# Kernel optimization log

Measured on AMD Instinct MI355X. Metric: run time of the kernel, lower is better.

Reference implementation:

```python
import jax, jax.numpy as jnp
import numpy as np

N = 100000
E = 1600000
IN_DIM, HIDDEN, OUT_DIM, HEADS = 256, 128, 64, 2
NEG_SLOPE = 0.2


def setup_inputs() -> dict:
    key = jax.random.key(0)
    ks = jax.random.split(key, 10)
    inv = lambda d: 1.0 / np.sqrt(d)
    return {
        "x": jax.random.normal(ks[0], (N, IN_DIM), dtype=jnp.float32),
        "edge_index": jax.random.randint(ks[1], (2, E), 0, N, dtype=jnp.int64),
        "W1": jax.random.normal(ks[2], (IN_DIM, HEADS * HIDDEN), dtype=jnp.float32) * inv(IN_DIM),
        "att_src1": jax.random.normal(ks[3], (HEADS, HIDDEN), dtype=jnp.float32) * inv(HIDDEN),
        "att_dst1": jax.random.normal(ks[4], (HEADS, HIDDEN), dtype=jnp.float32) * inv(HIDDEN),
        "b1": jnp.zeros((HIDDEN,), dtype=jnp.float32),
        "W2": jax.random.normal(ks[5], (HIDDEN, OUT_DIM), dtype=jnp.float32) * inv(HIDDEN),
        "att_src2": jax.random.normal(ks[6], (1, OUT_DIM), dtype=jnp.float32) * inv(OUT_DIM),
        "att_dst2": jax.random.normal(ks[7], (1, OUT_DIM), dtype=jnp.float32) * inv(OUT_DIM),
        "b2": jnp.zeros((OUT_DIM,), dtype=jnp.float32),
    }


def gat_conv(x, W, att_src, att_dst, bias, src, dst, heads, ch):
    # Linear transform: [N, H, C]
    h = (x @ W).reshape(N, heads, ch)
    # Per-node attention logits: [N, H]
    a_s = jnp.einsum("nhc,hc->nh", h, att_src)
    a_d = jnp.einsum("nhc,hc->nh", h, att_dst)
    # Edge-wise scores (self-loops already in src/dst): [E', H]
    e = jax.nn.leaky_relu(a_s[src] + a_d[dst], NEG_SLOPE)
    # Segment softmax over incoming edges of each dst node
    m = jax.ops.segment_max(e, dst, num_segments=N)
    alpha = jnp.exp(e - m[dst])
    denom = jax.ops.segment_sum(alpha, dst, num_segments=N)
    alpha = alpha / denom[dst]
    # Weighted scatter-add aggregation: [N, H, C]
    out = jax.ops.segment_sum(alpha[:, :, None] * h[src], dst, num_segments=N)
    # concat=False -> mean over heads, then bias
    return out.mean(axis=1) + bias


def reference(x, edge_index, W1, att_src1, att_dst1, b1, W2, att_src2, att_dst2, b2):
    # PyG GATConv default: add self-loops
    loop = jnp.arange(N, dtype=edge_index.dtype)
    src = jnp.concatenate([edge_index[0], loop])
    dst = jnp.concatenate([edge_index[1], loop])
    h = gat_conv(x, W1, att_src1, att_dst1, b1, src, dst, HEADS, HIDDEN)
    h = jax.nn.relu(h)  # dropout is identity in eval mode
    out = gat_conv(h, W2, att_src2, att_dst2, b2, src, dst, 1, OUT_DIM)
    return out
```

## Files before the change

### kernel.cpp

```cpp
#include <hip/hip_runtime.h>
#include <hip/hip_bf16.h>
#include <cstdint>
#include <cstddef>

#define IN_D 256
#define HID 128
#define OUT_D 64
#define NSLOPE 0.2f
#define SBCAP 20480

typedef __attribute__((ext_vector_type(8))) short bf16x8;
typedef __attribute__((ext_vector_type(4))) float f32x4;
typedef __attribute__((ext_vector_type(8))) unsigned short u16x8;
typedef unsigned short u16;

static inline int cdiv(long long a, long long b) { return (int)((a + b - 1) / b); }

__device__ __forceinline__ float lrelu(float v) { return v >= 0.f ? v : NSLOPE * v; }
__device__ __forceinline__ int imin(int a, int b) { return a < b ? a : b; }

__device__ __forceinline__ u16 f2bf(float f) {
  unsigned u = __float_as_uint(f);
  return (u16)((u + 0x7FFFu + ((u >> 16) & 1u)) >> 16);
}
__device__ __forceinline__ float bf2f(u16 h) {
  return __uint_as_float((unsigned)h << 16);
}

__global__ void k_prep(const float* __restrict__ W1, u16* __restrict__ WThi,
                       u16* __restrict__ WTlo, const float* __restrict__ W2,
                       u16* __restrict__ W2Thi, u16* __restrict__ W2Tlo) {
  int idx = blockIdx.x * 256 + threadIdx.x;
  if (idx < IN_D * IN_D) {
    int k = idx >> 8, n = idx & 255;
    float f = W1[idx];
    u16 h = f2bf(f);
    WThi[n * IN_D + k] = h;
    WTlo[n * IN_D + k] = f2bf(f - bf2f(h));
  }
  int idx2 = idx - IN_D * IN_D;
  if (idx2 >= 0 && idx2 < HID * OUT_D) {
    int k = idx2 >> 6, n = idx2 & 63;
    float f = W2[idx2];
    u16 h = f2bf(f);
    W2Thi[n * HID + k] = h;
    W2Tlo[n * HID + k] = f2bf(f - bf2f(h));
  }
}

__launch_bounds__(256)
__global__ void k_sort1(const int* __restrict__ ei, int E,
                        int* __restrict__ sbCount, int2* __restrict__ st1) {
  __shared__ int hist[128], gb[128], cur[128];
  int tid = threadIdx.x;
  if (tid < 128) hist[tid] = 0;
  __syncthreads();
  int base = blockIdx.x * 2048 + tid;
  int sv[8], dv[8]; bool vv[8];
  #pragma unroll
  for (int q = 0; q < 8; ++q) {
    int i = base + q * 256;
    vv[q] = i < E;
    int ic = vv[q] ? i : 0;
    sv[q] = ei[ic];
    dv[q] = ei[E + ic];
  }
  #pragma unroll
  for (int q = 0; q < 8; ++q)
    if (vv[q]) atomicAdd(&hist[dv[q] >> 10], 1);
  __syncthreads();
  if (tid < 128) {
    int h = hist[tid];
    gb[tid] = h ? atomicAdd(&sbCount[tid], h) : 0;
    cur[tid] = 0;
  }
  __syncthreads();
  #pragma unroll
  for (int q = 0; q < 8; ++q)
    if (vv[q]) {
      int sb = dv[q] >> 10;
      int r = atomicAdd(&cur[sb], 1);
      int slot = gb[sb] + r;
      if (slot < SBCAP) st1[(size_t)sb * SBCAP + slot] = make_int2(sv[q], dv[q]);
    }
}

__launch_bounds__(256)
__global__ void k_sort2(const int* __restrict__ sbCount, const int2* __restrict__ st1,
                        int* __restrict__ ro, int* __restrict__ col, int N) {
  __shared__ int hist2[1024], pref[1024], cur[1024];
  __shared__ int sc[256];
  __shared__ int gbaseS, cntS;
  int tid = threadIdx.x;
  int sb = blockIdx.x;
  int nb0 = sb << 10;
  if (tid == 0) {
    int g = 0;
    for (int b = 0; b < sb; ++b) g += imin(sbCount[b], SBCAP);
    gbaseS = g;
    cntS = imin(sbCount[sb], SBCAP);
  }
  for (int t = tid; t < 1024; t += 256) hist2[t] = 0;
  __syncthreads();
  int gbase = gbaseS, cnt = cntS;
  const int2* sp = st1 + (size_t)sb * SBCAP;
  for (int j = tid; j < cnt; j += 256) atomicAdd(&hist2[sp[j].y - nb0], 1);
  __syncthreads();
  int a0 = hist2[tid * 4], a1 = hist2[tid * 4 + 1],
      a2 = hist2[tid * 4 + 2], a3 = hist2[tid * 4 + 3];
  int s4 = a0 + a1 + a2 + a3;
  sc[tid] = s4; __syncthreads();
  for (int o = 1; o < 256; o <<= 1) {
    int add = (tid >= o) ? sc[tid - o] : 0;
    __syncthreads();
    sc[tid] += add;
    __syncthreads();
  }
  int eb = sc[tid] - s4;
  pref[tid * 4] = eb;
  pref[tid * 4 + 1] = eb + a0;
  pref[tid * 4 + 2] = eb + a0 + a1;
  pref[tid * 4 + 3] = eb + a0 + a1 + a2;
  __syncthreads();
  for (int t = tid; t < 1024; t += 256) {
    cur[t] = pref[t];
    int n = nb0 + t;
    if (n < N) ro[n] = gbase + pref[t];
  }
  if (sb == (int)gridDim.x - 1 && tid == 0) ro[N] = gbase + cnt;
  __syncthreads();
  for (int j = tid; j < cnt; j += 256) {
    int2 e = sp[j];
    int r = atomicAdd(&cur[e.y - nb0], 1);
    col[gbase + r] = e.x;
  }
}

__launch_bounds__(512)
__global__ void k_gemm1(const float* __restrict__ x, const u16* __restrict__ WThi,
                        const u16* __restrict__ WTlo,
                        const float* __restrict__ as1, const float* __restrict__ ad1,
                        u16* __restrict__ hb, float* __restrict__ a_s,
                        float* __restrict__ a_d, int N) {
  __shared__ u16 ldsb[2][10240];
  int tid = threadIdx.x;
  int w = tid >> 6, l = tid & 63;
  int l15 = l & 15, l4 = l >> 4;
  int rowbase = blockIdx.x * 128 + w * 16;
  int row = rowbase + l15;
  int rowc = (row < N) ? row : (N - 1);
  const float* xp = x + (size_t)rowc * IN_D + l4 * 8;

  f32x4 acc[16];
  #pragma unroll
  for (int t = 0; t < 16; ++t) acc[t] = (f32x4){0.f, 0.f, 0.f, 0.f};

  const int ridx = (l15 * 5 + l4) * 8;

  for (int kk = 0; kk < 8; ++kk) {
    __syncthreads();
    #pragma unroll
    for (int it = 0; it < 2; ++it) {
      int c = tid + it * 512;
      int n = c >> 2, ch = c & 3;
      size_t soff = (size_t)n * IN_D + kk * 32 + ch * 8;
      uint4 vh = *(const uint4*)(WThi + soff);
      uint4 vl = *(const uint4*)(WTlo + soff);
      int dsl = (n * 5 + ch) * 8;
      *(uint4*)&ldsb[0][dsl] = vh;
      *(uint4*)&ldsb[1][dsl] = vl;
    }
    __syncthreads();

    f32x4 v0 = *(const f32x4*)(xp + kk * 32);
    f32x4 v1 = *(const f32x4*)(xp + kk * 32 + 4);
    bf16x8 ah, al;
    #pragma unroll
    for (int j = 0; j < 4; ++j) {
      u16 h0 = f2bf(v0[j]);
      ah[j] = (short)h0; al[j] = (short)f2bf(v0[j] - bf2f(h0));
      u16 h1 = f2bf(v1[j]);
      ah[j + 4] = (short)h1; al[j + 4] = (short)f2bf(v1[j] - bf2f(h1));
    }
    #pragma unroll
    for (int t = 0; t < 16; ++t) {
      bf16x8 bh = *(const bf16x8*)&ldsb[0][ridx + t * 640];
      bf16x8 bl = *(const bf16x8*)&ldsb[1][ridx + t * 640];
      acc[t] = __builtin_amdgcn_mfma_f32_16x16x32_bf16(ah, bh, acc[t], 0, 0, 0);
      acc[t] = __builtin_amdgcn_mfma_f32_16x16x32_bf16(al, bh, acc[t], 0, 0, 0);
      acc[t] = __builtin_amdgcn_mfma_f32_16x16x32_bf16(ah, bl, acc[t], 0, 0, 0);
    }
  }

  #pragma unroll
  for (int r = 0; r < 4; ++r) {
    int rr = rowbase + l4 * 4 + r;
    if (rr < N) {
      u16* hp = hb + (size_t)rr * IN_D + l15;
      #pragma unroll
      for (int t = 0; t < 16; ++t) hp[t * 16] = f2bf(acc[t][r]);
    }
  }
  float asv[16], adv[16];
  #pragma unroll
  for (int t = 0; t < 16; ++t) { asv[t] = as1[t * 16 + l15]; adv[t] = ad1[t * 16 + l15]; }
  float ps0[4] = {}, ps1[4] = {}, pd0[4] = {}, pd1[4] = {};
  #pragma unroll
  for (int t = 0; t < 16; ++t) {
    #pragma unroll
    for (int r = 0; r < 4; ++r) {
      float v = acc[t][r];
      if (t < 8) { ps0[r] += v * asv[t]; pd0[r] += v * adv[t]; }
      else       { ps1[r] += v * asv[t]; pd1[r] += v * adv[t]; }
    }
  }
  #pragma unroll
  for (int r = 0; r < 4; ++r) {
    #pragma unroll
    for (int o = 1; o < 16; o <<= 1) {
      ps0[r] += __shfl_xor(ps0[r], o); ps1[r] += __shfl_xor(ps1[r], o);
      pd0[r] += __shfl_xor(pd0[r], o); pd1[r] += __shfl_xor(pd1[r], o);
    }
    int rr = rowbase + l4 * 4 + r;
    if (l15 == 0 && rr < N) {
      a_s[rr * 2] = ps0[r]; a_s[rr * 2 + 1] = ps1[r];
      a_d[rr * 2] = pd0[r]; a_d[rr * 2 + 1] = pd1[r];
    }
  }
}

__launch_bounds__(256)
__global__ void k_fagg1g2(const int* __restrict__ ro, const int* __restrict__ col,
                          const float* __restrict__ a_s, const float* __restrict__ a_d,
                          const u16* __restrict__ hb, const float* __restrict__ b1,
                          const u16* __restrict__ W2Thi, const u16* __restrict__ W2Tlo,
                          const float* __restrict__ as2, const float* __restrict__ ad2,
                          u16* __restrict__ h2b, float* __restrict__ a_s2,
                          float* __restrict__ a_d2, int N) {
  __shared__ float rowLds[16][132];
  __shared__ float red[2][16][4];
  int tid = threadIdx.x;
  int wid = tid >> 6, lane = tid & 63;
  int base = blockIdx.x * 16;

  int half = lane >> 5;
  int l5 = lane & 31;
  int head = l5 >> 4;

  for (int rr = 0; rr < 4; ++rr) {
    int ln = wid * 4 + rr;
    int n = base + ln;
    if (n >= N) { if (lane < 16) for (int q = 0; q < 8; ++q) rowLds[ln][lane * 8 + q] = 0.f; continue; }
    int beg = ro[n], end = ro[n + 1];
    float ad0 = a_d[2 * n], ad1 = a_d[2 * n + 1];
    float myAd = head ? ad1 : ad0;

    float sacc = 0.f;
    float accv[8] = {};
    if (half == 0) {
      float2 asn = *(const float2*)&a_s[2 * (size_t)n];
      float wv = __expf(lrelu((head ? asn.y : asn.x) + myAd));
      sacc = wv;
      const u16x8 hv = *(const u16x8*)&hb[(size_t)n * IN_D + l5 * 8];
      #pragma unroll
      for (int q = 0; q < 8; ++q) accv[q] = wv * bf2f(hv[q]);
    }
    #pragma unroll 4
    for (int j = beg; j < end; j += 2) {
      int jj = j + half;
      bool valid = jj < end;
      int sidx = col[valid ? jj : beg];
      float2 asv = *(const float2*)&a_s[2 * (size_t)sidx];
      float e = (head ? asv.y : asv.x) + myAd;
      float wv = __expf(lrelu(e));
      wv = valid ? wv : 0.f;
      sacc += wv;
      const u16x8 hv = *(const u16x8*)&hb[(size_t)sidx * IN_D + l5 * 8];
      #pragma unroll
      for (int q = 0; q < 8; ++q) accv[q] += wv * bf2f(hv[q]);
    }
    sacc += __shfl_xor(sacc, 32);
    float myScale = 0.5f / sacc;
    #pragma unroll
    for (int q = 0; q < 8; ++q) {
      accv[q] *= myScale;
      accv[q] += __shfl_xor(accv[q], 16);
      accv[q] += __shfl_xor(accv[q], 32);
    }
    if (lane < 16) {
      #pragma unroll
      for (int q = 0; q < 8; ++q) rowLds[ln][lane * 8 + q] = accv[q];
    }
  }
  __syncthreads();

  int l15 = lane & 15, l4 = lane >> 4;
  f32x4 acc2 = (f32x4){0.f, 0.f, 0.f, 0.f};
  #pragma unroll
  for (int kk = 0; kk < 4; ++kk) {
    int k0 = kk * 32 + l4 * 8;
    f32x4 bv0 = *(const f32x4*)(b1 + k0);
    f32x4 bv1 = *(const f32x4*)(b1 + k0 + 4);
    bf16x8 ah, al;
    #pragma unroll
    for (int j = 0; j < 4; ++j) {
      float u0 = rowLds[l15][k0 + j] + bv0[j]; u0 = (u0 > 0.f) ? u0 : 0.f;
      u16 h0 = f2bf(u0);
      ah[j] = (short)h0; al[j] = (short)f2bf(u0 - bf2f(h0));
      float u1 = rowLds[l15][k0 + 4 + j] + bv1[j]; u1 = (u1 > 0.f) ? u1 : 0.f;
      u16 h1 = f2bf(u1);
      ah[j + 4] = (short)h1; al[j + 4] = (short)f2bf(u1 - bf2f(h1));
    }
    size_t boff = (size_t)(wid * 16 + l15) * HID + k0;
    bf16x8 bh = *(const bf16x8*)(W2Thi + boff);
    bf16x8 bl = *(const bf16x8*)(W2Tlo + boff);
    acc2 = __builtin_amdgcn_mfma_f32_16x16x32_bf16(ah, bh, acc2, 0, 0, 0);
    acc2 = __builtin_amdgcn_mfma_f32_16x16x32_bf16(al, bh, acc2, 0, 0, 0);
    acc2 = __builtin_amdgcn_mfma_f32_16x16x32_bf16(ah, bl, acc2, 0, 0, 0);
  }

  float asv = as2[wid * 16 + l15], adv = ad2[wid * 16 + l15];
  float ps[4], pd[4];
  #pragma unroll
  for (int r = 0; r < 4; ++r) {
    int n = base + l4 * 4 + r;
    if (n < N) h2b[(size_t)n * OUT_D + wid * 16 + l15] = f2bf(acc2[r]);
    ps[r] = acc2[r] * asv; pd[r] = acc2[r] * adv;
    #pragma unroll
    for (int o = 1; o < 16; o <<= 1) { ps[r] += __shfl_xor(ps[r], o); pd[r] += __shfl_xor(pd[r], o); }
    if (l15 == 0) { red[0][l4 * 4 + r][wid] = ps[r]; red[1][l4 * 4 + r][wid] = pd[r]; }
  }
  __syncthreads();
  if (tid < 32) {
    int ln = tid >> 1, kind = tid & 1;
    int n = base + ln;
    if (n < N) {
      float v = red[kind][ln][0] + red[kind][ln][1] + red[kind][ln][2] + red[kind][ln][3];
      if (kind == 0) a_s2[n] = v; else a_d2[n] = v;
    }
  }
}

__launch_bounds__(256)
__global__ void k_fagg2(const int* __restrict__ ro, const int* __restrict__ col,
                        const float* __restrict__ a_s, const float* __restrict__ a_d,
                        const u16* __restrict__ h2b, const float* __restrict__ b2,
                        float* __restrict__ out, int N) {
  int gid = blockIdx.x * blockDim.x + threadIdx.x;
  int n = gid >> 6, lane = gid & 63;
  if (n >= N) return;
  int beg = ro[n], end = ro[n + 1];
  float ad = a_d[n];

  int g = lane >> 3, l3 = lane & 7;
  float sacc = 0.f;
  float accv[8] = {};
  if (g == 0) {
    float w = __expf(lrelu(a_s[n] + ad));
    sacc = w;
    const u16x8 hv = *(const u16x8*)&h2b[(size_t)n * OUT_D + l3 * 8];
    #pragma unroll
    for (int q = 0; q < 8; ++q) accv[q] = w * bf2f(hv[q]);
  }
  #pragma unroll 4
  for (int j = beg; j < end; j += 8) {
    int jj = j + g;
    bool valid = jj < end;
    int sidx = col[valid ? jj : beg];
    float w = __expf(lrelu(a_s[sidx] + ad));
    w = valid ? w : 0.f;
    sacc += w;
    const u16x8 hv = *(const u16x8*)&h2b[(size_t)sidx * OUT_D + l3 * 8];
    #pragma unroll
    for (int q = 0; q < 8; ++q) accv[q] += w * bf2f(hv[q]);
  }
  sacc += __shfl_xor(sacc, 8);
  sacc += __shfl_xor(sacc, 16);
  sacc += __shfl_xor(sacc, 32);
  float rcp = 1.f / sacc;
  #pragma unroll
  for (int q = 0; q < 8; ++q) {
    accv[q] *= rcp;
    accv[q] += __shfl_xor(accv[q], 8);
    accv[q] += __shfl_xor(accv[q], 16);
    accv[q] += __shfl_xor(accv[q], 32);
  }
  if (lane < 8) {
    float* op = out + (size_t)n * OUT_D + lane * 8;
    const float* bp = b2 + lane * 8;
    float4 o0 = {accv[0] + bp[0], accv[1] + bp[1], accv[2] + bp[2], accv[3] + bp[3]};
    float4 o1 = {accv[4] + bp[4], accv[5] + bp[5], accv[6] + bp[6], accv[7] + bp[7]};
    *(float4*)op = o0;
    *(float4*)(op + 4) = o1;
  }
}

extern "C" void kernel_launch(void* const* d_in, const int* in_sizes, int n_in,
                              void* d_out, int out_size, void* d_ws, size_t ws_size,
                              hipStream_t stream) {
  const float* x    = (const float*)d_in[0];
  const int*   ei   = (const int*)d_in[1];
  const float* W1   = (const float*)d_in[2];
  const float* as1w = (const float*)d_in[3];
  const float* ad1w = (const float*)d_in[4];
  const float* b1   = (const float*)d_in[5];
  const float* W2   = (const float*)d_in[6];
  const float* as2w = (const float*)d_in[7];
  const float* ad2w = (const float*)d_in[8];
  const float* b2   = (const float*)d_in[9];
  float* out = (float*)d_out;

  const int N   = in_sizes[0] / IN_D;
  const int E   = in_sizes[1] / 2;
  const int NSB = cdiv(N, 1024);

  float* ws = (float*)d_ws;
  size_t off = 0;
  u16*   hb1  = (u16*)(ws + off); off += (size_t)N * IN_D / 2;
  u16*   h2b  = (u16*)(ws + off); off += (size_t)N * OUT_D / 2;
  float* a_s1 = ws + off; off += (size_t)N * 2;
  float* a_d1 = ws + off; off += (size_t)N * 2;
  float* a_s2 = ws + off; off += N;
  float* a_d2 = ws + off; off += N;
  int*   sbCount = (int*)(ws + off); off += 128;
  int2*  st1  = (int2*)(ws + off); off += (size_t)NSB * SBCAP * 2;
  int*   ro   = (int*)(ws + off); off += (size_t)N + 1;
  int*   col  = (int*)(ws + off); off += E;
  u16*   WThi = (u16*)(ws + off); off += (IN_D * IN_D) / 2;
  u16*   WTlo = (u16*)(ws + off); off += (IN_D * IN_D) / 2;
  u16*   W2Thi = (u16*)(ws + off); off += (HID * OUT_D) / 2;
  u16*   W2Tlo = (u16*)(ws + off); off += (HID * OUT_D) / 2;

  hipMemsetAsync(sbCount, 0, 128 * sizeof(int), stream);

  k_prep<<<cdiv(IN_D * IN_D + HID * OUT_D, 256), 256, 0, stream>>>(
      W1, WThi, WTlo, W2, W2Thi, W2Tlo);

  k_sort1<<<cdiv(E, 2048), 256, 0, stream>>>(ei, E, sbCount, st1);
  k_sort2<<<NSB, 256, 0, stream>>>(sbCount, st1, ro, col, N);

  k_gemm1<<<cdiv(N, 128), 512, 0, stream>>>(x, WThi, WTlo, as1w, ad1w, hb1, a_s1, a_d1, N);

  k_fagg1g2<<<cdiv(N, 16), 256, 0, stream>>>(ro, col, a_s1, a_d1, hb1, b1,
                                             W2Thi, W2Tlo, as2w, ad2w, h2b, a_s2, a_d2, N);

  k_fagg2<<<cdiv((long long)N * 64, 256), 256, 0, stream>>>(ro, col, a_s2, a_d2, h2b, b2, out, N);
}
```

Before: 339.1 us.

## Merge edge bucketing into GEMM1 launch via interleaved heterogeneous blocks

Fuses the first edge-sort pass and the layer-1 GEMM into one launch whose blocks alternate between GEMM tiles and edge-bucketing tiles. The two jobs are independent, so the memory-bound scatter can overlap the MFMA-heavy GEMM and one kernel launch and its tail are removed. Sort blocks now use 512 threads with 4 edges each and reuse the GEMM's LDS buffer, but they still reserve the full GEMM LDS and register footprint, which may limit occupancy for the sort work.

Result: slower. 369.4 us (+8.9%).

```diff
diff --git a/kernel.cpp b/kernel.cpp
--- a/kernel.cpp
+++ b/kernel.cpp
@@ -48,41 +48,143 @@
   }
 }
 
-__launch_bounds__(256)
-__global__ void k_sort1(const int* __restrict__ ei, int E,
-                        int* __restrict__ sbCount, int2* __restrict__ st1) {
-  __shared__ int hist[128], gb[128], cur[128];
+__launch_bounds__(512)
+__global__ void k_gemm1sort(const float* __restrict__ x, const u16* __restrict__ WThi,
+                            const u16* __restrict__ WTlo,
+                            const float* __restrict__ as1, const float* __restrict__ ad1,
+                            u16* __restrict__ hb, float* __restrict__ a_s,
+                            float* __restrict__ a_d, int N,
+                            const int* __restrict__ ei, int E,
+                            int* __restrict__ sbCount, int2* __restrict__ st1,
+                            int G1, int G2) {
+  __shared__ u16 ldsb[2][10240];
+  int bid = blockIdx.x;
+  int m2 = (G1 < G2 ? G1 : G2) * 2;
+  int type, tb;
+  if (bid < m2) { type = bid & 1; tb = bid >> 1; }
+  else { int ex = bid - m2; type = (G1 > G2) ? 0 : 1; tb = m2 / 2 + ex; }
   int tid = threadIdx.x;
-  if (tid < 128) hist[tid] = 0;
-  __syncthreads();
-  int base = blockIdx.x * 2048 + tid;
-  int sv[8], dv[8]; bool vv[8];
-  #pragma unroll
-  for (int q = 0; q < 8; ++q) {
-    int i = base + q * 256;
-    vv[q] = i < E;
-    int ic = vv[q] ? i : 0;
-    sv[q] = ei[ic];
-    dv[q] = ei[E + ic];
-  }
-  #pragma unroll
-  for (int q = 0; q < 8; ++q)
-    if (vv[q]) atomicAdd(&hist[dv[q] >> 10], 1);
-  __syncthreads();
-  if (tid < 128) {
-    int h = hist[tid];
-    gb[tid] = h ? atomicAdd(&sbCount[tid], h) : 0;
-    cur[tid] = 0;
-  }
-  __syncthreads();
-  #pragma unroll
-  for (int q = 0; q < 8; ++q)
-    if (vv[q]) {
-      int sb = dv[q] >> 10;
-      int r = atomicAdd(&cur[sb], 1);
-      int slot = gb[sb] + r;
-      if (slot < SBCAP) st1[(size_t)sb * SBCAP + slot] = make_int2(sv[q], dv[q]);
-    }
+
+  if (type == 1) {
+    int* hist = (int*)&ldsb[0][0];
+    int* gb   = hist + 128;
+    int* cur  = hist + 256;
+    if (tid < 128) hist[tid] = 0;
+    __syncthreads();
+    int base = tb * 2048 + tid;
+    int sv[4], dv[4]; bool vv[4];
+    #pragma unroll
+    for (int q = 0; q < 4; ++q) {
+      int i = base + q * 512;
+      vv[q] = i < E;
+      int ic = vv[q] ? i : 0;
+      sv[q] = ei[ic];
+      dv[q] = ei[E + ic];
+    }
+    #pragma unroll
+    for (int q = 0; q < 4; ++q)
+      if (vv[q]) atomicAdd(&hist[dv[q] >> 10], 1);
+    __syncthreads();
+    if (tid < 128) {
+      int h = hist[tid];
+      gb[tid] = h ? atomicAdd(&sbCount[tid], h) : 0;
+      cur[tid] = 0;
+    }
+    __syncthreads();
+    #pragma unroll
+    for (int q = 0; q < 4; ++q)
+      if (vv[q]) {
+        int sb = dv[q] >> 10;
+        int r = atomicAdd(&cur[sb], 1);
+        int slot = gb[sb] + r;
+        if (slot < SBCAP) st1[(size_t)sb * SBCAP + slot] = make_int2(sv[q], dv[q]);
+      }
+    return;
+  }
+
+  int w = tid >> 6, l = tid & 63;
+  int l15 = l & 15, l4 = l >> 4;
+  int rowbase = tb * 128 + w * 16;
+  int row = rowbase + l15;
+  int rowc = (row < N) ? row : (N - 1);
+  const float* xp = x + (size_t)rowc * IN_D + l4 * 8;
+
+  f32x4 acc[16];
+  #pragma unroll
+  for (int t = 0; t < 16; ++t) acc[t] = (f32x4){0.f, 0.f, 0.f, 0.f};
+
+  const int ridx = (l15 * 5 + l4) * 8;
+
+  for (int kk = 0; kk < 8; ++kk) {
+    __syncthreads();
+    #pragma unroll
+    for (int it = 0; it < 2; ++it) {
+      int c = tid + it * 512;
+      int n = c >> 2, ch = c & 3;
+      size_t soff = (size_t)n * IN_D + kk * 32 + ch * 8;
+      uint4 vh = *(const uint4*)(WThi + soff);
+      uint4 vl = *(const uint4*)(WTlo + soff);
+      int dsl = (n * 5 + ch) * 8;
+      *(uint4*)&ldsb[0][dsl] = vh;
+      *(uint4*)&ldsb[1][dsl] = vl;
+    }
+    __syncthreads();
+
+    f32x4 v0 = *(const f32x4*)(xp + kk * 32);
+    f32x4 v1 = *(const f32x4*)(xp + kk * 32 + 4);
+    bf16x8 ah, al;
+    #pragma unroll
+    for (int j = 0; j < 4; ++j) {
+      u16 h0 = f2bf(v0[j]);
+      ah[j] = (short)h0; al[j] = (short)f2bf(v0[j] - bf2f(h0));
+      u16 h1 = f2bf(v1[j]);
+      ah[j + 4] = (short)h1; al[j + 4] = (short)f2bf(v1[j] - bf2f(h1));
+    }
+    #pragma unroll
+    for (int t = 0; t < 16; ++t) {
+      bf16x8 bh = *(const bf16x8*)&ldsb[0][ridx + t * 640];
+      bf16x8 bl = *(const bf16x8*)&ldsb[1][ridx + t * 640];
+      acc[t] = __builtin_amdgcn_mfma_f32_16x16x32_bf16(ah, bh, acc[t], 0, 0, 0);
+      acc[t] = __builtin_amdgcn_mfma_f32_16x16x32_bf16(al, bh, acc[t], 0, 0, 0);
+      acc[t] = __builtin_amdgcn_mfma_f32_16x16x32_bf16(ah, bl, acc[t], 0, 0, 0);
+    }
+  }
+
+  #pragma unroll
+  for (int r = 0; r < 4; ++r) {
+    int rr = rowbase + l4 * 4 + r;
+    if (rr < N) {
+      u16* hp = hb + (size_t)rr * IN_D + l15;
+      #pragma unroll
+      for (int t = 0; t < 16; ++t) hp[t * 16] = f2bf(acc[t][r]);
+    }
+  }
+  float asv[16], adv[16];
+  #pragma unroll
+  for (int t = 0; t < 16; ++t) { asv[t] = as1[t * 16 + l15]; adv[t] = ad1[t * 16 + l15]; }
+  float ps0[4] = {}, ps1[4] = {}, pd0[4] = {}, pd1[4] = {};
+  #pragma unroll
+  for (int t = 0; t < 16; ++t) {
+    #pragma unroll
+    for (int r = 0; r < 4; ++r) {
+      float v = acc[t][r];
+      if (t < 8) { ps0[r] += v * asv[t]; pd0[r] += v * adv[t]; }
+      else       { ps1[r] += v * asv[t]; pd1[r] += v * adv[t]; }
+    }
+  }
+  #pragma unroll
+  for (int r = 0; r < 4; ++r) {
+    #pragma unroll
+    for (int o = 1; o < 16; o <<= 1) {
+      ps0[r] += __shfl_xor(ps0[r], o); ps1[r] += __shfl_xor(ps1[r], o);
+      pd0[r] += __shfl_xor(pd0[r], o); pd1[r] += __shfl_xor(pd1[r], o);
+    }
+    int rr = rowbase + l4 * 4 + r;
+    if (l15 == 0 && rr < N) {
+      a_s[rr * 2] = ps0[r]; a_s[rr * 2 + 1] = ps1[r];
+      a_d[rr * 2] = pd0[r]; a_d[rr * 2 + 1] = pd1[r];
+    }
+  }
 }
 
 __launch_bounds__(256)
@@ -133,99 +235,6 @@
     int2 e = sp[j];
     int r = atomicAdd(&cur[e.y - nb0], 1);
     col[gbase + r] = e.x;
-  }
-}
-
-__launch_bounds__(512)
-__global__ void k_gemm1(const float* __restrict__ x, const u16* __restrict__ WThi,
-                        const u16* __restrict__ WTlo,
-                        const float* __restrict__ as1, const float* __restrict__ ad1,
-                        u16* __restrict__ hb, float* __restrict__ a_s,
-                        float* __restrict__ a_d, int N) {
-  __shared__ u16 ldsb[2][10240];
-  int tid = threadIdx.x;
-  int w = tid >> 6, l = tid & 63;
-  int l15 = l & 15, l4 = l >> 4;
-  int rowbase = blockIdx.x * 128 + w * 16;
-  int row = rowbase + l15;
-  int rowc = (row < N) ? row : (N - 1);
-  const float* xp = x + (size_t)rowc * IN_D + l4 * 8;
-
-  f32x4 acc[16];
-  #pragma unroll
-  for (int t = 0; t < 16; ++t) acc[t] = (f32x4){0.f, 0.f, 0.f, 0.f};
-
-  const int ridx = (l15 * 5 + l4) * 8;
-
-  for (int kk = 0; kk < 8; ++kk) {
-    __syncthreads();
-    #pragma unroll
-    for (int it = 0; it < 2; ++it) {
-      int c = tid + it * 512;
-      int n = c >> 2, ch = c & 3;
-      size_t soff = (size_t)n * IN_D + kk * 32 + ch * 8;
-      uint4 vh = *(const uint4*)(WThi + soff);
-      uint4 vl = *(const uint4*)(WTlo + soff);
-      int dsl = (n * 5 + ch) * 8;
-      *(uint4*)&ldsb[0][dsl] = vh;
-      *(uint4*)&ldsb[1][dsl] = vl;
-    }
-    __syncthreads();
-
-    f32x4 v0 = *(const f32x4*)(xp + kk * 32);
-    f32x4 v1 = *(const f32x4*)(xp + kk * 32 + 4);
-    bf16x8 ah, al;
-    #pragma unroll
-    for (int j = 0; j < 4; ++j) {
-      u16 h0 = f2bf(v0[j]);
-      ah[j] = (short)h0; al[j] = (short)f2bf(v0[j] - bf2f(h0));
-      u16 h1 = f2bf(v1[j]);
-      ah[j + 4] = (short)h1; al[j + 4] = (short)f2bf(v1[j] - bf2f(h1));
-    }
-    #pragma unroll
-    for (int t = 0; t < 16; ++t) {
-      bf16x8 bh = *(const bf16x8*)&ldsb[0][ridx + t * 640];
-      bf16x8 bl = *(const bf16x8*)&ldsb[1][ridx + t * 640];
-      acc[t] = __builtin_amdgcn_mfma_f32_16x16x32_bf16(ah, bh, acc[t], 0, 0, 0);
-      acc[t] = __builtin_amdgcn_mfma_f32_16x16x32_bf16(al, bh, acc[t], 0, 0, 0);
-      acc[t] = __builtin_amdgcn_mfma_f32_16x16x32_bf16(ah, bl, acc[t], 0, 0, 0);
-    }
-  }
-
-  #pragma unroll
-  for (int r = 0; r < 4; ++r) {
-    int rr = rowbase + l4 * 4 + r;
-    if (rr < N) {
-      u16* hp = hb + (size_t)rr * IN_D + l15;
-      #pragma unroll
-      for (int t = 0; t < 16; ++t) hp[t * 16] = f2bf(acc[t][r]);
-    }
-  }
-  float asv[16], adv[16];
-  #pragma unroll
-  for (int t = 0; t < 16; ++t) { asv[t] = as1[t * 16 + l15]; adv[t] = ad1[t * 16 + l15]; }
-  float ps0[4] = {}, ps1[4] = {}, pd0[4] = {}, pd1[4] = {};
-  #pragma unroll
-  for (int t = 0; t < 16; ++t) {
-    #pragma unroll
-    for (int r = 0; r < 4; ++r) {
-      float v = acc[t][r];
-      if (t < 8) { ps0[r] += v * asv[t]; pd0[r] += v * adv[t]; }
-      else       { ps1[r] += v * asv[t]; pd1[r] += v * adv[t]; }
-    }
-  }
-  #pragma unroll
-  for (int r = 0; r < 4; ++r) {
-    #pragma unroll
-    for (int o = 1; o < 16; o <<= 1) {
-      ps0[r] += __shfl_xor(ps0[r], o); ps1[r] += __shfl_xor(ps1[r], o);
-      pd0[r] += __shfl_xor(pd0[r], o); pd1[r] += __shfl_xor(pd1[r], o);
-    }
-    int rr = rowbase + l4 * 4 + r;
-    if (l15 == 0 && rr < N) {
-      a_s[rr * 2] = ps0[r]; a_s[rr * 2 + 1] = ps1[r];
-      a_d[rr * 2] = pd0[r]; a_d[rr * 2 + 1] = pd1[r];
-    }
   }
 }
 
@@ -436,10 +445,12 @@
   k_prep<<<cdiv(IN_D * IN_D + HID * OUT_D, 256), 256, 0, stream>>>(
       W1, WThi, WTlo, W2, W2Thi, W2Tlo);
 
-  k_sort1<<<cdiv(E, 2048), 256, 0, stream>>>(ei, E, sbCount, st1);
+  const int G1 = cdiv(N, 128);
+  const int G2 = cdiv(E, 2048);
+  k_gemm1sort<<<G1 + G2, 512, 0, stream>>>(x, WThi, WTlo, as1w, ad1w, hb1, a_s1, a_d1, N,
+                                           ei, E, sbCount, st1, G1, G2);
+
   k_sort2<<<NSB, 256, 0, stream>>>(sbCount, st1, ro, col, N);
-
-  k_gemm1<<<cdiv(N, 128), 512, 0, stream>>>(x, WThi, WTlo, as1w, ad1w, hb1, a_s1, a_d1, N);
 
   k_fagg1g2<<<cdiv(N, 16), 256, 0, stream>>>(ro, col, a_s1, a_d1, hb1, b1,
                                              W2Thi, W2Tlo, as2w, ad2w, h2b, a_s2, a_d2, N);
```
